# Kernel tuning notes

Measured on AMD Instinct MI355X. Metric: run time of the kernel, lower is better.

The kernel has to match this reference:

```python
import jax, jax.numpy as jnp
import numpy as np

N0, N1, N2, N3 = 600000, 100000, 20000, 4096
E0, E1, E2 = 1500000, 200000, 40960
D_IN, D_H, D_OUT = 100, 256, 47


def setup_inputs() -> dict:
    key = jax.random.key(0)
    ks = jax.random.split(key, 16)
    inp = {
        "x": jax.random.normal(ks[0], (N0, D_IN), jnp.float32),
        "ei0_src": jax.random.randint(ks[1], (E0,), 0, N0, jnp.int32),
        "ei0_dst": jax.random.randint(ks[2], (E0,), 0, N1, jnp.int32),
        "ei1_src": jax.random.randint(ks[3], (E1,), 0, N1, jnp.int32),
        "ei1_dst": jax.random.randint(ks[4], (E1,), 0, N2, jnp.int32),
        "ei2_src": jax.random.randint(ks[5], (E2,), 0, N2, jnp.int32),
        "ei2_dst": jax.random.randint(ks[6], (E2,), 0, N3, jnp.int32),
        "Wl0": jax.random.normal(ks[7], (D_IN, D_H), jnp.float32) * 0.1,
        "Wr0": jax.random.normal(ks[8], (D_IN, D_H), jnp.float32) * 0.1,
        "b0": jnp.zeros((D_H,), jnp.float32),
        "Wl1": jax.random.normal(ks[9], (D_H, D_H), jnp.float32) * 0.06,
        "Wr1": jax.random.normal(ks[10], (D_H, D_H), jnp.float32) * 0.06,
        "b1": jnp.zeros((D_H,), jnp.float32),
        "Wl2": jax.random.normal(ks[11], (D_H, D_OUT), jnp.float32) * 0.06,
        "Wr2": jax.random.normal(ks[12], (D_H, D_OUT), jnp.float32) * 0.06,
        "b2": jnp.zeros((D_OUT,), jnp.float32),
    }
    return inp


def _sage_layer(x_src, x_tgt, src, dst, n_tgt, Wl, Wr, b):
    # PyG SAGEConv (mean aggr): out = lin_l(mean_{j in N(i)} x_j) + lin_r(x_i)
    msgs = x_src[src]                                   # [E, d] gather
    s = jax.ops.segment_sum(msgs, dst, num_segments=n_tgt)
    cnt = jax.ops.segment_sum(jnp.ones((src.shape[0],), x_src.dtype), dst,
                              num_segments=n_tgt)[:, None]
    mean = s / jnp.maximum(cnt, 1.0)
    return mean @ Wl + x_tgt @ Wr + b


def reference(x, ei0_src, ei0_dst, ei1_src, ei1_dst, ei2_src, ei2_dst,
              Wl0, Wr0, b0, Wl1, Wr1, b1, Wl2, Wr2, b2):
    h = _sage_layer(x, x[:N1], ei0_src, ei0_dst, N1, Wl0, Wr0, b0)
    h = jax.nn.relu(h)  # dropout is identity in eval mode
    h = _sage_layer(h, h[:N2], ei1_src, ei1_dst, N2, Wl1, Wr1, b1)
    h = jax.nn.relu(h)
    h = _sage_layer(h, h[:N3], ei2_src, ei2_dst, N3, Wl2, Wr2, b2)
    return jax.nn.log_softmax(h, axis=-1)
```

## Files before the change

kernel.cpp:

```cpp
#include <hip/hip_runtime.h>

#define NN0 600000
#define NN1 100000
#define NN2 20000
#define NN3 4096
#define EE0 1500000
#define EE1 200000
#define EE2 40960
#define DIN 100
#define DH  256
#define DOUT 47
#define NTOT (NN1 + NN2 + NN3)

#define RNG 16384
#define CH0 32768
#define NC0 46
#define R0  7
#define CH1 16384
#define NC1 13
#define R1  2
#define CH2 8192
#define NC2 5
#define R2  1
#define HL0 (NC0 * R0)
#define HL1 (NC1 * R1)
#define HL2 (NC2 * R2)
#define HLT (HL0 + HL1 + HL2)
#define NGMAX 46
#define CONVB 1536

#define NB0 98
#define NB1 20
#define NB2 4
#define NBT 122

#define HB0 5860
#define HB1 782
#define HB2 160
#define HBE (HB0 + HB1 + HB2)

typedef unsigned int uint;
typedef unsigned short ushort;
typedef __attribute__((ext_vector_type(8))) short bhalf8;
typedef __attribute__((ext_vector_type(4))) float f32x4;

union U16B {
    uint2  u2[2];
    uint4  u4;
    bhalf8 s8;
    ushort us[8];
};

__device__ __forceinline__ ushort f2bf(float f) {
    uint u = __float_as_uint(f);
    uint r = (u + 0x7FFFu + ((u >> 16) & 1u)) >> 16;
    return (ushort)r;
}
__device__ __forceinline__ float bf2f(uint bits16) {
    return __uint_as_float(bits16 << 16);
}

__global__ __launch_bounds__(1024)
void hist_conv(const int* __restrict__ e0d, const int* __restrict__ e1d,
               const int* __restrict__ e2d, int* __restrict__ cntp,
               int* __restrict__ pos0, int* __restrict__ pos1,
               int* __restrict__ pos2,
               const float* __restrict__ x, ushort* __restrict__ xb,
               long long n4) {
    __shared__ int lcnt[RNG];
    int b = blockIdx.x, tid = threadIdx.x;
    if (b >= HLT) {
        long long cb = b - HLT;
        for (long long t = cb * 1024 + tid; t < n4; t += (long long)CONVB * 1024) {
            float4 v = *reinterpret_cast<const float4*>(x + t * 4);
            uint2 o;
            o.x = (uint)f2bf(v.x) | ((uint)f2bf(v.y) << 16);
            o.y = (uint)f2bf(v.z) | ((uint)f2bf(v.w) << 16);
            *reinterpret_cast<uint2*>(xb + t * 4) = o;
        }
        return;
    }
    const int* dstp; int E, CH, c, r, nbase, layerN;
    int* pos;
    if (b < HL0) {
        dstp = e0d; E = EE0; CH = CH0; c = b / R0; r = b % R0;
        nbase = 0; layerN = NN1; pos = pos0;
    } else if (b < HL0 + HL1) {
        int bb = b - HL0;
        dstp = e1d; E = EE1; CH = CH1; c = bb / R1; r = bb % R1;
        nbase = NN1; layerN = NN2; pos = pos1;
    } else {
        int bb = b - HL0 - HL1;
        dstp = e2d; E = EE2; CH = CH2; c = bb; r = 0;
        nbase = NN1 + NN2; layerN = NN3; pos = pos2;
    }
    for (int i = tid; i < RNG; i += 1024) lcnt[i] = 0;
    __syncthreads();
    int rbase = r * RNG;
    long long ebase = (long long)c * CH;
    for (int i = tid; i < CH; i += 1024) {
        int e = (int)(ebase + i);
        if (e < E) {
            int d = dstp[e];
            unsigned li = (unsigned)(d - rbase);
            if (li < RNG) pos[e] = atomicAdd(&lcnt[li], 1);
        }
    }
    __syncthreads();
    for (int i = tid; i < RNG; i += 1024) {
        int node = rbase + i;
        if (node < layerN)
            cntp[(size_t)c * NTOT + nbase + node] = lcnt[i];
    }
}

__device__ __forceinline__ void pack_one(const float* B, int K, int N, int NB,
                                         ushort* out, int bid, int l) {
    int kstep = bid / NB;
    int c = bid % NB;
    U16B v;
    #pragma unroll
    for (int j = 0; j < 8; ++j) {
        int k = kstep * 32 + ((l >> 4) << 3) + j;
        int col = (c << 4) | (l & 15);
        float f = (k < K && col < N) ? B[(size_t)k * N + col] : 0.0f;
        v.us[j] = f2bf(f);
    }
    *reinterpret_cast<bhalf8*>(out + ((size_t)bid * 64 + l) * 8) = v.s8;
}

__global__ __launch_bounds__(256)
void pack_all(const float* __restrict__ Wl0, const float* __restrict__ Wr0,
              const float* __restrict__ Wl1, const float* __restrict__ Wr1,
              const float* __restrict__ Wl2, const float* __restrict__ Wr2,
              ushort* Bp0l, ushort* Bp0r, ushort* Bp1l, ushort* Bp1r,
              ushort* Bp2l, ushort* Bp2r) {
    int bid = blockIdx.x * 4 + (threadIdx.x >> 6);
    int l = threadIdx.x & 63;
    if (bid < 64)       pack_one(Wl0, DIN, DH,  16, Bp0l, bid,       l);
    else if (bid < 128) pack_one(Wr0, DIN, DH,  16, Bp0r, bid - 64,  l);
    else if (bid < 256) pack_one(Wl1, DH,  DH,  16, Bp1l, bid - 128, l);
    else if (bid < 384) pack_one(Wr1, DH,  DH,  16, Bp1r, bid - 256, l);
    else if (bid < 408) pack_one(Wl2, DH,  DOUT, 3, Bp2l, bid - 384, l);
    else if (bid < 432) pack_one(Wr2, DH,  DOUT, 3, Bp2r, bid - 408, l);
}

__global__ __launch_bounds__(256)
void combine_parts(int* __restrict__ cntp, int* __restrict__ cntAll) {
    int i = blockIdx.x * 256 + threadIdx.x;
    if (i >= NTOT) return;
    int ng = (i < NN1) ? NC0 : (i < NN1 + NN2) ? NC1 : NC2;
    int run = 0;
    for (int g = 0; g < ng; ++g) {
        size_t idx = (size_t)g * NTOT + i;
        int v = cntp[idx];
        cntp[idx] = run;
        run += v;
    }
    cntAll[i] = run;
}


__device__ __forceinline__ void layer_of(int b, int& lb, int& n, int& po, int& cb) {
    if (b < NB0)      { lb = b;        n = NN1; po = 0;         cb = 0; }
    else if (b < NB0 + NB1) { lb = b - NB0;  n = NN2; po = NB0; cb = NN1; }
    else              { lb = b - NB0 - NB1; n = NN3; po = NB0 + NB1; cb = NN1 + NN2; }
}

__global__ void scan1f(const int* __restrict__ cntAll, int* __restrict__ part) {
    int lb, n, po, cb;
    layer_of(blockIdx.x, lb, n, po, cb);
    __shared__ int s[256];
    int base = lb * 1024;
    int sum = 0;
    for (int i = threadIdx.x; i < 1024; i += 256) {
        int idx = base + i;
        sum += (idx < n) ? cntAll[cb + idx] : 0;
    }
    s[threadIdx.x] = sum;
    __syncthreads();
    for (int off = 128; off; off >>= 1) {
        if (threadIdx.x < off) s[threadIdx.x] += s[threadIdx.x + off];
        __syncthreads();
    }
    if (threadIdx.x == 0) part[po + lb] = s[0];
}

__global__ void scan2f(int* part) {
    __shared__ int s[128];
    int t = threadIdx.x;
    int seg = (t < NB0) ? 0 : (t < NB0 + NB1) ? 1 : (t < NBT) ? 2 : 3;
    int v = (t < NBT) ? part[t] : 0;
    s[t] = v;
    __syncthreads();
    for (int off = 1; off < 128; off <<= 1) {
        int add = 0;
        if (t >= off) {
            int u = t - off;
            int segu = (u < NB0) ? 0 : (u < NB0 + NB1) ? 1 : (u < NBT) ? 2 : 3;
            if (segu == seg) add = s[u];
        }
        __syncthreads();
        s[t] += add;
        __syncthreads();
    }
    if (t < NBT) part[t] = s[t] - v;
}

__global__ void scan3f(const int* __restrict__ cntAll, const int* __restrict__ part,
                       int* __restrict__ rp0, int* __restrict__ rp1,
                       int* __restrict__ rp2) {
    int lb, n, po, cb;
    layer_of(blockIdx.x, lb, n, po, cb);
    int* row_ptr;
    if (cb == 0)        row_ptr = rp0;
    else if (cb == NN1) row_ptr = rp1;
    else                row_ptr = rp2;

    __shared__ int s[256];
    int base = lb * 1024;
    int v[4];
    int sum = 0;
    #pragma unroll
    for (int j = 0; j < 4; ++j) {
        int idx = base + threadIdx.x * 4 + j;
        v[j] = (idx < n) ? cntAll[cb + idx] : 0;
        sum += v[j];
    }
    s[threadIdx.x] = sum;
    __syncthreads();
    for (int off = 1; off < 256; off <<= 1) {
        int t = (threadIdx.x >= off) ? s[threadIdx.x - off] : 0;
        __syncthreads();
        s[threadIdx.x] += t;
        __syncthreads();
    }
    int off0 = part[po + lb] + s[threadIdx.x] - sum;
    #pragma unroll
    for (int j = 0; j < 4; ++j) {
        int idx = base + threadIdx.x * 4 + j;
        if (idx < n) {
            row_ptr[idx] = off0;
            off0 += v[j];
            if (idx == n - 1) row_ptr[n] = off0;
        }
    }
}

__global__ __launch_bounds__(256)
void place_all(const int* __restrict__ e0s, const int* __restrict__ e0d,
               const int* __restrict__ e1s, const int* __restrict__ e1d,
               const int* __restrict__ e2s, const int* __restrict__ e2d,
               const int* __restrict__ pos0, const int* __restrict__ pos1,
               const int* __restrict__ pos2, const int* __restrict__ cntp,
               const int* __restrict__ rp0, const int* __restrict__ rp1,
               const int* __restrict__ rp2,
               int* __restrict__ eidx0, int* __restrict__ eidx1,
               int* __restrict__ eidx2) {
    int b = blockIdx.x;
    int tid = threadIdx.x;
    if (b < HB0) {
        int e = b * 256 + tid;
        if (e < EE0) {
            int d = e0d[e];
            int g = e >> 15;
            int p = rp0[d] + cntp[(size_t)g * NTOT + d] + pos0[e];
            eidx0[p] = e0s[e];
        }
    } else if (b < HB0 + HB1) {
        int e = (b - HB0) * 256 + tid;
        if (e < EE1) {
            int d = e1d[e];
            int g = e >> 14;
            int p = rp1[d] + cntp[(size_t)g * NTOT + NN1 + d] + pos1[e];
            eidx1[p] = e1s[e];
        }
    } else {
        int e = (b - HB0 - HB1) * 256 + tid;
        if (e < EE2) {
            int d = e2d[e];
            int g = e >> 13;
            int p = rp2[d] + cntp[(size_t)g * NTOT + NN1 + NN2 + d] + pos2[e];
            eidx2[p] = e2s[e];
        }
    }
}


__global__ __launch_bounds__(256)
void agg100_b(const ushort* __restrict__ xb, const int* __restrict__ rp,
              const int* __restrict__ eidx, ushort* __restrict__ out, int nNodes) {
    int node = blockIdx.x * 4 + (threadIdx.x >> 6);
    if (node >= nNodes) return;
    int l = threadIdx.x & 63;
    bool act = l < 50;
    int beg = rp[node], end = rp[node + 1];
    float a0 = 0.f, a1 = 0.f;
    int j = beg;
    for (; j + 3 < end; j += 4) {
        int s0 = eidx[j], s1 = eidx[j + 1], s2 = eidx[j + 2], s3 = eidx[j + 3];
        if (act) {
            uint v0 = *reinterpret_cast<const uint*>(xb + (size_t)s0 * DIN + l * 2);
            uint v1 = *reinterpret_cast<const uint*>(xb + (size_t)s1 * DIN + l * 2);
            uint v2 = *reinterpret_cast<const uint*>(xb + (size_t)s2 * DIN + l * 2);
            uint v3 = *reinterpret_cast<const uint*>(xb + (size_t)s3 * DIN + l * 2);
            a0 += bf2f(v0 & 0xffffu) + bf2f(v1 & 0xffffu) + bf2f(v2 & 0xffffu) + bf2f(v3 & 0xffffu);
            a1 += bf2f(v0 >> 16) + bf2f(v1 >> 16) + bf2f(v2 >> 16) + bf2f(v3 >> 16);
        }
    }
    for (; j < end; ++j) {
        int s0 = eidx[j];
        if (act) {
            uint v0 = *reinterpret_cast<const uint*>(xb + (size_t)s0 * DIN + l * 2);
            a0 += bf2f(v0 & 0xffffu);
            a1 += bf2f(v0 >> 16);
        }
    }
    float inv = 1.0f / fmaxf((float)(end - beg), 1.0f);
    if (act) {
        uint o = (uint)f2bf(a0 * inv) | ((uint)f2bf(a1 * inv) << 16);
        *reinterpret_cast<uint*>(out + (size_t)node * DIN + l * 2) = o;
    }
}

__global__ __launch_bounds__(256)
void agg256_b(const ushort* __restrict__ h, const int* __restrict__ rp,
              const int* __restrict__ eidx, ushort* __restrict__ out, int nNodes) {
    int node = blockIdx.x * 4 + (threadIdx.x >> 6);
    if (node >= nNodes) return;
    int l = threadIdx.x & 63;
    int beg = rp[node], end = rp[node + 1];
    float a0 = 0.f, a1 = 0.f, a2 = 0.f, a3 = 0.f;
    int j = beg;
    for (; j + 3 < end; j += 4) {
        int s0 = eidx[j], s1 = eidx[j + 1], s2 = eidx[j + 2], s3 = eidx[j + 3];
        uint2 v0 = *reinterpret_cast<const uint2*>(h + (size_t)s0 * DH + l * 4);
        uint2 v1 = *reinterpret_cast<const uint2*>(h + (size_t)s1 * DH + l * 4);
        uint2 v2 = *reinterpret_cast<const uint2*>(h + (size_t)s2 * DH + l * 4);
        uint2 v3 = *reinterpret_cast<const uint2*>(h + (size_t)s3 * DH + l * 4);
        a0 += bf2f(v0.x & 0xffffu) + bf2f(v1.x & 0xffffu) + bf2f(v2.x & 0xffffu) + bf2f(v3.x & 0xffffu);
        a1 += bf2f(v0.x >> 16)     + bf2f(v1.x >> 16)     + bf2f(v2.x >> 16)     + bf2f(v3.x >> 16);
        a2 += bf2f(v0.y & 0xffffu) + bf2f(v1.y & 0xffffu) + bf2f(v2.y & 0xffffu) + bf2f(v3.y & 0xffffu);
        a3 += bf2f(v0.y >> 16)     + bf2f(v1.y >> 16)     + bf2f(v2.y >> 16)     + bf2f(v3.y >> 16);
    }
    for (; j < end; ++j) {
        int s0 = eidx[j];
        uint2 v0 = *reinterpret_cast<const uint2*>(h + (size_t)s0 * DH + l * 4);
        a0 += bf2f(v0.x & 0xffffu);
        a1 += bf2f(v0.x >> 16);
        a2 += bf2f(v0.y & 0xffffu);
        a3 += bf2f(v0.y >> 16);
    }
    float inv = 1.0f / fmaxf((float)(end - beg), 1.0f);
    uint2 o;
    o.x = (uint)f2bf(a0 * inv) | ((uint)f2bf(a1 * inv) << 16);
    o.y = (uint)f2bf(a2 * inv) | ((uint)f2bf(a3 * inv) << 16);
    *reinterpret_cast<uint2*>(out + (size_t)node * DH + l * 4) = o;
}

template <int RELU, int OUTBF, int A2F32>
__global__ __launch_bounds__(256)
void gemm_dual(const ushort* __restrict__ A1, int K1, int S1, int str1,
               const void* __restrict__ A2, int K2, int S2, int str2,
               const ushort* __restrict__ B1p, const ushort* __restrict__ B2p,
               const float* __restrict__ bias, void* __restrict__ Cv,
               int M, int N, int NB, int NBW, int Cstride) {
    __shared__ ushort At[2][2048];

    const int tid = threadIdx.x;
    const int w = tid >> 6;
    const int l = tid & 63;
    const int m0 = blockIdx.x * 64;
    const int S = S1 + S2;

    f32x4 acc[4][4];
    #pragma unroll
    for (int m = 0; m < 4; ++m)
        #pragma unroll
        for (int i = 0; i < 4; ++i)
            acc[m][i] = f32x4{0.f, 0.f, 0.f, 0.f};

    auto stage = [&](int s, int buf) {
        int r  = tid >> 2;
        int kc = tid & 3;
        int row = m0 + r;
        U16B v;
        v.u4.x = v.u4.y = v.u4.z = v.u4.w = 0u;
        if (s < S1) {
            int k = s * 32 + (kc << 3);
            if (row < M && k < K1) {
                const ushort* p = A1 + (size_t)row * str1 + k;
                v.u2[0] = *reinterpret_cast<const uint2*>(p);
                v.u2[1] = *reinterpret_cast<const uint2*>(p + 4);
                if (k + 8 > K1) {
                    #pragma unroll
                    for (int j = 0; j < 8; ++j)
                        if (k + j >= K1) v.us[j] = 0;
                }
            }
        } else {
            int ks = s - S1;
            int k = ks * 32 + (kc << 3);
            if (row < M && k < K2) {
                if (A2F32) {
                    const float* p = (const float*)A2 + (size_t)row * str2 + k;
                    float4 f0 = *reinterpret_cast<const float4*>(p);
                    float4 f1 = *reinterpret_cast<const float4*>(p + 4);
                    v.us[0] = f2bf(f0.x); v.us[1] = f2bf(f0.y);
                    v.us[2] = f2bf(f0.z); v.us[3] = f2bf(f0.w);
                    v.us[4] = f2bf(f1.x); v.us[5] = f2bf(f1.y);
                    v.us[6] = f2bf(f1.z); v.us[7] = f2bf(f1.w);
                } else {
                    const ushort* p = (const ushort*)A2 + (size_t)row * str2 + k;
                    v.u2[0] = *reinterpret_cast<const uint2*>(p);
                    v.u2[1] = *reinterpret_cast<const uint2*>(p + 4);
                }
                if (k + 8 > K2) {
                    #pragma unroll
                    for (int j = 0; j < 8; ++j)
                        if (k + j >= K2) v.us[j] = 0;
                }
            }
        }
        int slot = ((r >> 4) << 6) | (r & 15) | (kc << 4);
        *reinterpret_cast<bhalf8*>(&At[buf][slot * 8]) = v.s8;
    };

    stage(0, 0);
    __syncthreads();

    for (int s = 0; s < S; ++s) {
        int buf = s & 1;
        if (s + 1 < S) stage(s + 1, buf ^ 1);

        const ushort* Bp; int ks;
        if (s < S1) { Bp = B1p; ks = s; }
        else        { Bp = B2p; ks = s - S1; }

        bhalf8 a[4];
        #pragma unroll
        for (int m = 0; m < 4; ++m)
            a[m] = *reinterpret_cast<bhalf8*>(&At[buf][((m << 6) | l) * 8]);

        #pragma unroll
        for (int i = 0; i < 4; ++i) {
            if (i < NBW) {
                int c = w * NBW + i;
                if (c < NB) {
                    bhalf8 b = *reinterpret_cast<const bhalf8*>(
                        Bp + ((size_t)(ks * NB + c) * 64 + l) * 8);
                    #pragma unroll
                    for (int m = 0; m < 4; ++m)
                        acc[m][i] = __builtin_amdgcn_mfma_f32_16x16x32_bf16(
                            a[m], b, acc[m][i], 0, 0, 0);
                }
            }
        }
        __syncthreads();
    }

    #pragma unroll
    for (int i = 0; i < 4; ++i) {
        if (i >= NBW) continue;
        int c = w * NBW + i;
        if (c >= NB) continue;
        int col = (c << 4) | (l & 15);
        if (col >= N) continue;
        float bb = bias[col];
        #pragma unroll
        for (int m = 0; m < 4; ++m) {
            #pragma unroll
            for (int e = 0; e < 4; ++e) {
                int row = m0 + (m << 4) + ((l >> 4) << 2) + e;
                if (row < M) {
                    float v = acc[m][i][e] + bb;
                    if (RELU) v = fmaxf(v, 0.0f);
                    if (OUTBF)
                        ((ushort*)Cv)[(size_t)row * Cstride + col] = f2bf(v);
                    else
                        ((float*)Cv)[(size_t)row * Cstride + col] = v;
                }
            }
        }
    }
}

__global__ void log_softmax_47(const float* __restrict__ z, float* __restrict__ out) {
    int row = blockIdx.x;
    int lane = threadIdx.x;
    float v = (lane < DOUT) ? z[(size_t)row * DOUT + lane] : -INFINITY;
    float m = v;
    #pragma unroll
    for (int off = 32; off; off >>= 1) m = fmaxf(m, __shfl_xor(m, off));
    float e = (lane < DOUT) ? expf(v - m) : 0.0f;
    float s = e;
    #pragma unroll
    for (int off = 32; off; off >>= 1) s += __shfl_xor(s, off);
    if (lane < DOUT) out[(size_t)row * DOUT + lane] = v - m - logf(s);
}

extern "C" void kernel_launch(void* const* d_in, const int* in_sizes, int n_in,
                              void* d_out, int out_size, void* d_ws, size_t ws_size,
                              hipStream_t stream) {
    const float* x   = (const float*)d_in[0];
    const int* e0s   = (const int*)d_in[1];
    const int* e0d   = (const int*)d_in[2];
    const int* e1s   = (const int*)d_in[3];
    const int* e1d   = (const int*)d_in[4];
    const int* e2s   = (const int*)d_in[5];
    const int* e2d   = (const int*)d_in[6];
    const float* Wl0 = (const float*)d_in[7];
    const float* Wr0 = (const float*)d_in[8];
    const float* b0  = (const float*)d_in[9];
    const float* Wl1 = (const float*)d_in[10];
    const float* Wr1 = (const float*)d_in[11];
    const float* b1  = (const float*)d_in[12];
    const float* Wl2 = (const float*)d_in[13];
    const float* Wr2 = (const float*)d_in[14];
    const float* b2  = (const float*)d_in[15];

    char* ws = (char*)d_ws;
    size_t off = 0;
    auto alloc = [&](size_t bytes) -> void* {
        void* p = ws + off;
        off += (bytes + 255) & ~(size_t)255;
        return p;
    };

    ushort* agg0b = (ushort*)alloc((size_t)NN1 * DIN * 2);
    ushort* h1    = (ushort*)alloc((size_t)NN1 * DH * 2);
    ushort* agg1b = (ushort*)alloc((size_t)NN2 * DH * 2);
    ushort* h2    = (ushort*)alloc((size_t)NN2 * DH * 2);
    ushort* agg2b = (ushort*)alloc((size_t)NN3 * DH * 2);
    float*  z     = (float*)alloc((size_t)NN3 * DOUT * 4);

    ushort* Bp0l = (ushort*)alloc((size_t)4 * 16 * 64 * 8 * 2);
    ushort* Bp0r = (ushort*)alloc((size_t)4 * 16 * 64 * 8 * 2);
    ushort* Bp1l = (ushort*)alloc((size_t)8 * 16 * 64 * 8 * 2);
    ushort* Bp1r = (ushort*)alloc((size_t)8 * 16 * 64 * 8 * 2);
    ushort* Bp2l = (ushort*)alloc((size_t)8 * 3 * 64 * 8 * 2);
    ushort* Bp2r = (ushort*)alloc((size_t)8 * 3 * 64 * 8 * 2);

    int* cntp   = (int*)alloc((size_t)NGMAX * NTOT * 4);
    int* cntAll = (int*)alloc((size_t)NTOT * 4);
    int* pos0   = (int*)alloc((size_t)EE0 * 4);
    int* pos1   = (int*)alloc((size_t)EE1 * 4);
    int* pos2   = (int*)alloc((size_t)EE2 * 4);
    int* rp0    = (int*)alloc((size_t)(NN1 + 1) * 4);
    int* eidx0  = (int*)alloc((size_t)EE0 * 4);
    int* rp1    = (int*)alloc((size_t)(NN2 + 1) * 4);
    int* eidx1  = (int*)alloc((size_t)EE1 * 4);
    int* rp2    = (int*)alloc((size_t)(NN3 + 1) * 4);
    int* eidx2  = (int*)alloc((size_t)EE2 * 4);
    int* part   = (int*)alloc(256 * 4);
    ushort* xb  = (ushort*)alloc((size_t)NN0 * DIN * 2 + 256);

    {
        long long n4 = (long long)NN0 * DIN / 4;
        hist_conv<<<HLT + CONVB, 1024, 0, stream>>>(
            e0d, e1d, e2d, cntp, pos0, pos1, pos2, x, xb, n4);
    }
    pack_all<<<108, 256, 0, stream>>>(Wl0, Wr0, Wl1, Wr1, Wl2, Wr2,
                                      Bp0l, Bp0r, Bp1l, Bp1r, Bp2l, Bp2r);

    combine_parts<<<(NTOT + 255) / 256, 256, 0, stream>>>(cntp, cntAll);
    scan1f<<<NBT, 256, 0, stream>>>(cntAll, part);
    scan2f<<<1, 128, 0, stream>>>(part);
    scan3f<<<NBT, 256, 0, stream>>>(cntAll, part, rp0, rp1, rp2);

    place_all<<<HBE, 256, 0, stream>>>(e0s, e0d, e1s, e1d, e2s, e2d,
                                       pos0, pos1, pos2, cntp,
                                       rp0, rp1, rp2, eidx0, eidx1, eidx2);

    agg100_b<<<(NN1 + 3) / 4, 256, 0, stream>>>(xb, rp0, eidx0, agg0b, NN1);
    gemm_dual<1, 1, 0><<<(NN1 + 63) / 64, 256, 0, stream>>>(
        agg0b, DIN, 4, DIN, (const void*)xb, DIN, 4, DIN, Bp0l, Bp0r, b0, h1,
        NN1, DH, 16, 4, DH);

    agg256_b<<<(NN2 + 3) / 4, 256, 0, stream>>>(h1, rp1, eidx1, agg1b, NN2);
    gemm_dual<1, 1, 0><<<(NN2 + 63) / 64, 256, 0, stream>>>(
        agg1b, DH, 8, DH, (const void*)h1, DH, 8, DH, Bp1l, Bp1r, b1, h2,
        NN2, DH, 16, 4, DH);

    agg256_b<<<(NN3 + 3) / 4, 256, 0, stream>>>(h2, rp2, eidx2, agg2b, NN3);
    gemm_dual<0, 0, 0><<<(NN3 + 63) / 64, 256, 0, stream>>>(
        agg2b, DH, 8, DH, (const void*)h2, DH, 8, DH, Bp2l, Bp2r, b2, z,
        NN3, DOUT, 3, 1, DOUT);

    log_softmax_47<<<NN3, 64, 0, stream>>>(z, (float*)d_out);
}
```

Baseline: 443.7 us.

## Fuse preprocessing kernels, move x conversion into placement, widen gathers

Weight packing moves into the histogram kernel. The fp32-to-bf16 conversion of x moves into the edge-placement kernel so it overlaps scatter work. The combine, partial-scan and block-offset scan kernels are merged into two launches, which drops the single-block scan2 kernel because each block redundantly sums the earlier partials. The aggregation loops use 8 gathered rows per iteration, and agg100 uses 32-lane half-waves with 4 features per lane. Together these remove several launches and serial dependencies, and raise memory-level parallelism in the gathers, at the cost of more register pressure and redundant per-block prefix work.

```diff
diff --git a/kernel.cpp b/kernel.cpp
--- a/kernel.cpp
+++ b/kernel.cpp
@@ -27,7 +27,7 @@
 #define HL2 (NC2 * R2)
 #define HLT (HL0 + HL1 + HL2)
 #define NGMAX 46
-#define CONVB 1536
+#define PACKB 27
 
 #define NB0 98
 #define NB1 20
@@ -38,6 +38,7 @@
 #define HB1 782
 #define HB2 160
 #define HBE (HB0 + HB1 + HB2)
+#define CONVB 3072
 
 typedef unsigned int uint;
 typedef unsigned short ushort;
@@ -60,24 +61,42 @@
     return __uint_as_float(bits16 << 16);
 }
 
+__device__ __forceinline__ void pack_one(const float* B, int K, int N, int NB,
+                                         ushort* out, int bid, int l) {
+    int kstep = bid / NB;
+    int c = bid % NB;
+    U16B v;
+    #pragma unroll
+    for (int j = 0; j < 8; ++j) {
+        int k = kstep * 32 + ((l >> 4) << 3) + j;
+        int col = (c << 4) | (l & 15);
+        float f = (k < K && col < N) ? B[(size_t)k * N + col] : 0.0f;
+        v.us[j] = f2bf(f);
+    }
+    *reinterpret_cast<bhalf8*>(out + ((size_t)bid * 64 + l) * 8) = v.s8;
+}
+
 __global__ __launch_bounds__(1024)
-void hist_conv(const int* __restrict__ e0d, const int* __restrict__ e1d,
+void hist_pack(const int* __restrict__ e0d, const int* __restrict__ e1d,
                const int* __restrict__ e2d, int* __restrict__ cntp,
                int* __restrict__ pos0, int* __restrict__ pos1,
                int* __restrict__ pos2,
-               const float* __restrict__ x, ushort* __restrict__ xb,
-               long long n4) {
+               const float* __restrict__ Wl0, const float* __restrict__ Wr0,
+               const float* __restrict__ Wl1, const float* __restrict__ Wr1,
+               const float* __restrict__ Wl2, const float* __restrict__ Wr2,
+               ushort* Bp0l, ushort* Bp0r, ushort* Bp1l, ushort* Bp1r,
+               ushort* Bp2l, ushort* Bp2r) {
     __shared__ int lcnt[RNG];
     int b = blockIdx.x, tid = threadIdx.x;
     if (b >= HLT) {
-        long long cb = b - HLT;
-        for (long long t = cb * 1024 + tid; t < n4; t += (long long)CONVB * 1024) {
-            float4 v = *reinterpret_cast<const float4*>(x + t * 4);
-            uint2 o;
-            o.x = (uint)f2bf(v.x) | ((uint)f2bf(v.y) << 16);
-            o.y = (uint)f2bf(v.z) | ((uint)f2bf(v.w) << 16);
-            *reinterpret_cast<uint2*>(xb + t * 4) = o;
-        }
+        int bid = (b - HLT) * 16 + (tid >> 6);
+        int l = tid & 63;
+        if (bid < 64)       pack_one(Wl0, DIN, DH,  16, Bp0l, bid,       l);
+        else if (bid < 128) pack_one(Wr0, DIN, DH,  16, Bp0r, bid - 64,  l);
+        else if (bid < 256) pack_one(Wl1, DH,  DH,  16, Bp1l, bid - 128, l);
+        else if (bid < 384) pack_one(Wr1, DH,  DH,  16, Bp1r, bid - 256, l);
+        else if (bid < 408) pack_one(Wl2, DH,  DOUT, 3, Bp2l, bid - 384, l);
+        else if (bid < 432) pack_one(Wr2, DH,  DOUT, 3, Bp2r, bid - 408, l);
         return;
     }
     const int* dstp; int E, CH, c, r, nbase, layerN;
@@ -114,69 +133,37 @@
     }
 }
 
-__device__ __forceinline__ void pack_one(const float* B, int K, int N, int NB,
-                                         ushort* out, int bid, int l) {
-    int kstep = bid / NB;
-    int c = bid % NB;
-    U16B v;
-    #pragma unroll
-    for (int j = 0; j < 8; ++j) {
-        int k = kstep * 32 + ((l >> 4) << 3) + j;
-        int col = (c << 4) | (l & 15);
-        float f = (k < K && col < N) ? B[(size_t)k * N + col] : 0.0f;
-        v.us[j] = f2bf(f);
-    }
-    *reinterpret_cast<bhalf8*>(out + ((size_t)bid * 64 + l) * 8) = v.s8;
-}
-
-__global__ __launch_bounds__(256)
-void pack_all(const float* __restrict__ Wl0, const float* __restrict__ Wr0,
-              const float* __restrict__ Wl1, const float* __restrict__ Wr1,
-              const float* __restrict__ Wl2, const float* __restrict__ Wr2,
-              ushort* Bp0l, ushort* Bp0r, ushort* Bp1l, ushort* Bp1r,
-              ushort* Bp2l, ushort* Bp2r) {
-    int bid = blockIdx.x * 4 + (threadIdx.x >> 6);
-    int l = threadIdx.x & 63;
-    if (bid < 64)       pack_one(Wl0, DIN, DH,  16, Bp0l, bid,       l);
-    else if (bid < 128) pack_one(Wr0, DIN, DH,  16, Bp0r, bid - 64,  l);
-    else if (bid < 256) pack_one(Wl1, DH,  DH,  16, Bp1l, bid - 128, l);
-    else if (bid < 384) pack_one(Wr1, DH,  DH,  16, Bp1r, bid - 256, l);
-    else if (bid < 408) pack_one(Wl2, DH,  DOUT, 3, Bp2l, bid - 384, l);
-    else if (bid < 432) pack_one(Wr2, DH,  DOUT, 3, Bp2r, bid - 408, l);
-}
-
-__global__ __launch_bounds__(256)
-void combine_parts(int* __restrict__ cntp, int* __restrict__ cntAll) {
-    int i = blockIdx.x * 256 + threadIdx.x;
-    if (i >= NTOT) return;
-    int ng = (i < NN1) ? NC0 : (i < NN1 + NN2) ? NC1 : NC2;
-    int run = 0;
-    for (int g = 0; g < ng; ++g) {
-        size_t idx = (size_t)g * NTOT + i;
-        int v = cntp[idx];
-        cntp[idx] = run;
-        run += v;
-    }
-    cntAll[i] = run;
-}
-
-
 __device__ __forceinline__ void layer_of(int b, int& lb, int& n, int& po, int& cb) {
     if (b < NB0)      { lb = b;        n = NN1; po = 0;         cb = 0; }
     else if (b < NB0 + NB1) { lb = b - NB0;  n = NN2; po = NB0; cb = NN1; }
     else              { lb = b - NB0 - NB1; n = NN3; po = NB0 + NB1; cb = NN1 + NN2; }
 }
 
-__global__ void scan1f(const int* __restrict__ cntAll, int* __restrict__ part) {
+__global__ __launch_bounds__(256)
+void combScan1(int* __restrict__ cntp, int* __restrict__ cntAll,
+               int* __restrict__ part) {
     int lb, n, po, cb;
     layer_of(blockIdx.x, lb, n, po, cb);
-    __shared__ int s[256];
+    int ng = (cb == 0) ? NC0 : (cb == NN1) ? NC1 : NC2;
     int base = lb * 1024;
     int sum = 0;
-    for (int i = threadIdx.x; i < 1024; i += 256) {
-        int idx = base + i;
-        sum += (idx < n) ? cntAll[cb + idx] : 0;
-    }
+    #pragma unroll
+    for (int jj = 0; jj < 4; ++jj) {
+        int idx = base + threadIdx.x * 4 + jj;
+        if (idx < n) {
+            int i = cb + idx;
+            int run = 0;
+            for (int g = 0; g < ng; ++g) {
+                size_t id = (size_t)g * NTOT + i;
+                int v = cntp[id];
+                cntp[id] = run;
+                run += v;
+            }
+            cntAll[i] = run;
+            sum += run;
+        }
+    }
+    __shared__ int s[256];
     s[threadIdx.x] = sum;
     __syncthreads();
     for (int off = 128; off; off >>= 1) {
@@ -186,30 +173,9 @@
     if (threadIdx.x == 0) part[po + lb] = s[0];
 }
 
-__global__ void scan2f(int* part) {
-    __shared__ int s[128];
-    int t = threadIdx.x;
-    int seg = (t < NB0) ? 0 : (t < NB0 + NB1) ? 1 : (t < NBT) ? 2 : 3;
-    int v = (t < NBT) ? part[t] : 0;
-    s[t] = v;
-    __syncthreads();
-    for (int off = 1; off < 128; off <<= 1) {
-        int add = 0;
-        if (t >= off) {
-            int u = t - off;
-            int segu = (u < NB0) ? 0 : (u < NB0 + NB1) ? 1 : (u < NBT) ? 2 : 3;
-            if (segu == seg) add = s[u];
-        }
-        __syncthreads();
-        s[t] += add;
-        __syncthreads();
-    }
-    if (t < NBT) part[t] = s[t] - v;
-}
-
-__global__ void scan3f(const int* __restrict__ cntAll, const int* __restrict__ part,
-                       int* __restrict__ rp0, int* __restrict__ rp1,
-                       int* __restrict__ rp2) {
+__global__ __launch_bounds__(256)
+void scan3L(const int* __restrict__ cntAll, const int* __restrict__ part,
+            int* __restrict__ rp0, int* __restrict__ rp1, int* __restrict__ rp2) {
     int lb, n, po, cb;
     layer_of(blockIdx.x, lb, n, po, cb);
     int* row_ptr;
@@ -217,7 +183,18 @@
     else if (cb == NN1) row_ptr = rp1;
     else                row_ptr = rp2;
 
+    __shared__ int partL[NBT];
     __shared__ int s[256];
+    __shared__ int segOff;
+    for (int i = threadIdx.x; i < NBT; i += 256) partL[i] = part[i];
+    __syncthreads();
+    if (threadIdx.x == 0) {
+        int acc = 0;
+        for (int k = 0; k < lb; ++k) acc += partL[po + k];
+        segOff = acc;
+    }
+    __syncthreads();
+
     int base = lb * 1024;
     int v[4];
     int sum = 0;
@@ -235,7 +212,7 @@
         s[threadIdx.x] += t;
         __syncthreads();
     }
-    int off0 = part[po + lb] + s[threadIdx.x] - sum;
+    int off0 = segOff + s[threadIdx.x] - sum;
     #pragma unroll
     for (int j = 0; j < 4; ++j) {
         int idx = base + threadIdx.x * 4 + j;
@@ -248,15 +225,17 @@
 }
 
 __global__ __launch_bounds__(256)
-void place_all(const int* __restrict__ e0s, const int* __restrict__ e0d,
-               const int* __restrict__ e1s, const int* __restrict__ e1d,
-               const int* __restrict__ e2s, const int* __restrict__ e2d,
-               const int* __restrict__ pos0, const int* __restrict__ pos1,
-               const int* __restrict__ pos2, const int* __restrict__ cntp,
-               const int* __restrict__ rp0, const int* __restrict__ rp1,
-               const int* __restrict__ rp2,
-               int* __restrict__ eidx0, int* __restrict__ eidx1,
-               int* __restrict__ eidx2) {
+void place_conv(const int* __restrict__ e0s, const int* __restrict__ e0d,
+                const int* __restrict__ e1s, const int* __restrict__ e1d,
+                const int* __restrict__ e2s, const int* __restrict__ e2d,
+                const int* __restrict__ pos0, const int* __restrict__ pos1,
+                const int* __restrict__ pos2, const int* __restrict__ cntp,
+                const int* __restrict__ rp0, const int* __restrict__ rp1,
+                const int* __restrict__ rp2,
+                int* __restrict__ eidx0, int* __restrict__ eidx1,
+                int* __restrict__ eidx2,
+                const float* __restrict__ x, ushort* __restrict__ xb,
+                long long n4) {
     int b = blockIdx.x;
     int tid = threadIdx.x;
     if (b < HB0) {
@@ -275,7 +254,7 @@
             int p = rp1[d] + cntp[(size_t)g * NTOT + NN1 + d] + pos1[e];
             eidx1[p] = e1s[e];
         }
-    } else {
+    } else if (b < HBE) {
         int e = (b - HB0 - HB1) * 256 + tid;
         if (e < EE2) {
             int d = e2d[e];
@@ -283,6 +262,15 @@
             int p = rp2[d] + cntp[(size_t)g * NTOT + NN1 + NN2 + d] + pos2[e];
             eidx2[p] = e2s[e];
         }
+    } else {
+        long long cb = b - HBE;
+        for (long long t = cb * 256 + tid; t < n4; t += (long long)CONVB * 256) {
+            float4 v = *reinterpret_cast<const float4*>(x + t * 4);
+            uint2 o;
+            o.x = (uint)f2bf(v.x) | ((uint)f2bf(v.y) << 16);
+            o.y = (uint)f2bf(v.z) | ((uint)f2bf(v.w) << 16);
+            *reinterpret_cast<uint2*>(xb + t * 4) = o;
+        }
     }
 }
 
@@ -290,36 +278,47 @@
 __global__ __launch_bounds__(256)
 void agg100_b(const ushort* __restrict__ xb, const int* __restrict__ rp,
               const int* __restrict__ eidx, ushort* __restrict__ out, int nNodes) {
-    int node = blockIdx.x * 4 + (threadIdx.x >> 6);
+    int node = blockIdx.x * 8 + (threadIdx.x >> 5);
     if (node >= nNodes) return;
-    int l = threadIdx.x & 63;
-    bool act = l < 50;
+    int hl = threadIdx.x & 31;
+    bool act = hl < 25;
     int beg = rp[node], end = rp[node + 1];
-    float a0 = 0.f, a1 = 0.f;
+    float a0 = 0.f, a1 = 0.f, a2 = 0.f, a3 = 0.f;
     int j = beg;
-    for (; j + 3 < end; j += 4) {
-        int s0 = eidx[j], s1 = eidx[j + 1], s2 = eidx[j + 2], s3 = eidx[j + 3];
+    for (; j + 7 < end; j += 8) {
+        int sidx[8];
+        #pragma unroll
+        for (int q = 0; q < 8; ++q) sidx[q] = eidx[j + q];
         if (act) {
-            uint v0 = *reinterpret_cast<const uint*>(xb + (size_t)s0 * DIN + l * 2);
-            uint v1 = *reinterpret_cast<const uint*>(xb + (size_t)s1 * DIN + l * 2);
-            uint v2 = *reinterpret_cast<const uint*>(xb + (size_t)s2 * DIN + l * 2);
-            uint v3 = *reinterpret_cast<const uint*>(xb + (size_t)s3 * DIN + l * 2);
-            a0 += bf2f(v0 & 0xffffu) + bf2f(v1 & 0xffffu) + bf2f(v2 & 0xffffu) + bf2f(v3 & 0xffffu);
-            a1 += bf2f(v0 >> 16) + bf2f(v1 >> 16) + bf2f(v2 >> 16) + bf2f(v3 >> 16);
+            uint2 vv[8];
+            #pragma unroll
+            for (int q = 0; q < 8; ++q)
+                vv[q] = *reinterpret_cast<const uint2*>(xb + (size_t)sidx[q] * DIN + hl * 4);
+            #pragma unroll
+            for (int q = 0; q < 8; ++q) {
+                a0 += bf2f(vv[q].x & 0xffffu);
+                a1 += bf2f(vv[q].x >> 16);
+                a2 += bf2f(vv[q].y & 0xffffu);
+                a3 += bf2f(vv[q].y >> 16);
+            }
         }
     }
     for (; j < end; ++j) {
         int s0 = eidx[j];
         if (act) {
-            uint v0 = *reinterpret_cast<const uint*>(xb + (size_t)s0 * DIN + l * 2);
-            a0 += bf2f(v0 & 0xffffu);
-            a1 += bf2f(v0 >> 16);
+            uint2 v0 = *reinterpret_cast<const uint2*>(xb + (size_t)s0 * DIN + hl * 4);
+            a0 += bf2f(v0.x & 0xffffu);
+            a1 += bf2f(v0.x >> 16);
+            a2 += bf2f(v0.y & 0xffffu);
+            a3 += bf2f(v0.y >> 16);
         }
     }
     float inv = 1.0f / fmaxf((float)(end - beg), 1.0f);
     if (act) {
-        uint o = (uint)f2bf(a0 * inv) | ((uint)f2bf(a1 * inv) << 16);
-        *reinterpret_cast<uint*>(out + (size_t)node * DIN + l * 2) = o;
+        uint2 o;
+        o.x = (uint)f2bf(a0 * inv) | ((uint)f2bf(a1 * inv) << 16);
+        o.y = (uint)f2bf(a2 * inv) | ((uint)f2bf(a3 * inv) << 16);
+        *reinterpret_cast<uint2*>(out + (size_t)node * DIN + hl * 4) = o;
     }
 }
 
@@ -332,16 +331,21 @@
     int beg = rp[node], end = rp[node + 1];
     float a0 = 0.f, a1 = 0.f, a2 = 0.f, a3 = 0.f;
     int j = beg;
-    for (; j + 3 < end; j += 4) {
-        int s0 = eidx[j], s1 = eidx[j + 1], s2 = eidx[j + 2], s3 = eidx[j + 3];
-        uint2 v0 = *reinterpret_cast<const uint2*>(h + (size_t)s0 * DH + l * 4);
-        uint2 v1 = *reinterpret_cast<const uint2*>(h + (size_t)s1 * DH + l * 4);
-        uint2 v2 = *reinterpret_cast<const uint2*>(h + (size_t)s2 * DH + l * 4);
-        uint2 v3 = *reinterpret_cast<const uint2*>(h + (size_t)s3 * DH + l * 4);
-        a0 += bf2f(v0.x & 0xffffu) + bf2f(v1.x & 0xffffu) + bf2f(v2.x & 0xffffu) + bf2f(v3.x & 0xffffu);
-        a1 += bf2f(v0.x >> 16)     + bf2f(v1.x >> 16)     + bf2f(v2.x >> 16)     + bf2f(v3.x >> 16);
-        a2 += bf2f(v0.y & 0xffffu) + bf2f(v1.y & 0xffffu) + bf2f(v2.y & 0xffffu) + bf2f(v3.y & 0xffffu);
-        a3 += bf2f(v0.y >> 16)     + bf2f(v1.y >> 16)     + bf2f(v2.y >> 16)     + bf2f(v3.y >> 16);
+    for (; j + 7 < end; j += 8) {
+        int sidx[8];
+        #pragma unroll
+        for (int q = 0; q < 8; ++q) sidx[q] = eidx[j + q];
+        uint2 vv[8];
+        #pragma unroll
+        for (int q = 0; q < 8; ++q)
+            vv[q] = *reinterpret_cast<const uint2*>(h + (size_t)sidx[q] * DH + l * 4);
+        #pragma unroll
+        for (int q = 0; q < 8; ++q) {
+            a0 += bf2f(vv[q].x & 0xffffu);
+            a1 += bf2f(vv[q].x >> 16);
+            a2 += bf2f(vv[q].y & 0xffffu);
+            a3 += bf2f(vv[q].y >> 16);
+        }
     }
     for (; j < end; ++j) {
         int s0 = eidx[j];
@@ -358,10 +362,10 @@
     *reinterpret_cast<uint2*>(out + (size_t)node * DH + l * 4) = o;
 }
 
-template <int RELU, int OUTBF, int A2F32>
+template <int RELU, int OUTBF>
 __global__ __launch_bounds__(256)
 void gemm_dual(const ushort* __restrict__ A1, int K1, int S1, int str1,
-               const void* __restrict__ A2, int K2, int S2, int str2,
+               const ushort* __restrict__ A2, int K2, int S2, int str2,
                const ushort* __restrict__ B1p, const ushort* __restrict__ B2p,
                const float* __restrict__ bias, void* __restrict__ Cv,
                int M, int N, int NB, int NBW, int Cstride) {
@@ -381,45 +385,23 @@
             acc[m][i] = f32x4{0.f, 0.f, 0.f, 0.f};
 
     auto stage = [&](int s, int buf) {
+        const ushort* A; int str, Keff, ks;
+        if (s < S1) { A = A1; str = str1; Keff = K1; ks = s; }
+        else        { A = A2; str = str2; Keff = K2; ks = s - S1; }
         int r  = tid >> 2;
         int kc = tid & 3;
         int row = m0 + r;
+        int k = ks * 32 + (kc << 3);
         U16B v;
         v.u4.x = v.u4.y = v.u4.z = v.u4.w = 0u;
-        if (s < S1) {
-            int k = s * 32 + (kc << 3);
-            if (row < M && k < K1) {
-                const ushort* p = A1 + (size_t)row * str1 + k;
-                v.u2[0] = *reinterpret_cast<const uint2*>(p);
-                v.u2[1] = *reinterpret_cast<const uint2*>(p + 4);
-                if (k + 8 > K1) {
-                    #pragma unroll
-                    for (int j = 0; j < 8; ++j)
-                        if (k + j >= K1) v.us[j] = 0;
-                }
-            }
-        } else {
-            int ks = s - S1;
-            int k = ks * 32 + (kc << 3);
-            if (row < M && k < K2) {
-                if (A2F32) {
-                    const float* p = (const float*)A2 + (size_t)row * str2 + k;
-                    float4 f0 = *reinterpret_cast<const float4*>(p);
-                    float4 f1 = *reinterpret_cast<const float4*>(p + 4);
-                    v.us[0] = f2bf(f0.x); v.us[1] = f2bf(f0.y);
-                    v.us[2] = f2bf(f0.z); v.us[3] = f2bf(f0.w);
-                    v.us[4] = f2bf(f1.x); v.us[5] = f2bf(f1.y);
-                    v.us[6] = f2bf(f1.z); v.us[7] = f2bf(f1.w);
-                } else {
-                    const ushort* p = (const ushort*)A2 + (size_t)row * str2 + k;
-                    v.u2[0] = *reinterpret_cast<const uint2*>(p);
-                    v.u2[1] = *reinterpret_cast<const uint2*>(p + 4);
-                }
-                if (k + 8 > K2) {
-                    #pragma unroll
-                    for (int j = 0; j < 8; ++j)
-                        if (k + j >= K2) v.us[j] = 0;
-                }
+        if (row < M && k < Keff) {
+            const ushort* p = A + (size_t)row * str + k;
+            v.u2[0] = *reinterpret_cast<const uint2*>(p);
+            v.u2[1] = *reinterpret_cast<const uint2*>(p + 4);
+            if (k + 8 > Keff) {
+                #pragma unroll
+                for (int j = 0; j < 8; ++j)
+                    if (k + j >= Keff) v.us[j] = 0;
             }
         }
         int slot = ((r >> 4) << 6) | (r & 15) | (kc << 4);
@@ -555,36 +537,34 @@
     int* part   = (int*)alloc(256 * 4);
     ushort* xb  = (ushort*)alloc((size_t)NN0 * DIN * 2 + 256);
 
+    hist_pack<<<HLT + PACKB, 1024, 0, stream>>>(
+        e0d, e1d, e2d, cntp, pos0, pos1, pos2,
+        Wl0, Wr0, Wl1, Wr1, Wl2, Wr2,
+        Bp0l, Bp0r, Bp1l, Bp1r, Bp2l, Bp2r);
+
+    combScan1<<<NBT, 256, 0, stream>>>(cntp, cntAll, part);
+    scan3L<<<NBT, 256, 0, stream>>>(cntAll, part, rp0, rp1, rp2);
+
     {
         long long n4 = (long long)NN0 * DIN / 4;
-        hist_conv<<<HLT + CONVB, 1024, 0, stream>>>(
-            e0d, e1d, e2d, cntp, pos0, pos1, pos2, x, xb, n4);
-    }
-    pack_all<<<108, 256, 0, stream>>>(Wl0, Wr0, Wl1, Wr1, Wl2, Wr2,
-                                      Bp0l, Bp0r, Bp1l, Bp1r, Bp2l, Bp2r);
-
-    combine_parts<<<(NTOT + 255) / 256, 256, 0, stream>>>(cntp, cntAll);
-    scan1f<<<NBT, 256, 0, stream>>>(cntAll, part);
-    scan2f<<<1, 128, 0, stream>>>(part);
-    scan3f<<<NBT, 256, 0, stream>>>(cntAll, part, rp0, rp1, rp2);
-
-    place_all<<<HBE, 256, 0, stream>>>(e0s, e0d, e1s, e1d, e2s, e2d,
-                                       pos0, pos1, pos2, cntp,
-                                       rp0, rp1, rp2, eidx0, eidx1, eidx2);
-
-    agg100_b<<<(NN1 + 3) / 4, 256, 0, stream>>>(xb, rp0, eidx0, agg0b, NN1);
-    gemm_dual<1, 1, 0><<<(NN1 + 63) / 64, 256, 0, stream>>>(
-        agg0b, DIN, 4, DIN, (const void*)xb, DIN, 4, DIN, Bp0l, Bp0r, b0, h1,
+        place_conv<<<HBE + CONVB, 256, 0, stream>>>(
+            e0s, e0d, e1s, e1d, e2s, e2d, pos0, pos1, pos2, cntp,
+            rp0, rp1, rp2, eidx0, eidx1, eidx2, x, xb, n4);
+    }
+
+    agg100_b<<<(NN1 + 7) / 8, 256, 0, stream>>>(xb, rp0, eidx0, agg0b, NN1);
+    gemm_dual<1, 1><<<(NN1 + 63) / 64, 256, 0, stream>>>(
+        agg0b, DIN, 4, DIN, xb, DIN, 4, DIN, Bp0l, Bp0r, b0, h1,
         NN1, DH, 16, 4, DH);
 
     agg256_b<<<(NN2 + 3) / 4, 256, 0, stream>>>(h1, rp1, eidx1, agg1b, NN2);
-    gemm_dual<1, 1, 0><<<(NN2 + 63) / 64, 256, 0, stream>>>(
-        agg1b, DH, 8, DH, (const void*)h1, DH, 8, DH, Bp1l, Bp1r, b1, h2,
+    gemm_dual<1, 1><<<(NN2 + 63) / 64, 256, 0, stream>>>(
+        agg1b, DH, 8, DH, h1, DH, 8, DH, Bp1l, Bp1r, b1, h2,
         NN2, DH, 16, 4, DH);
 
     agg256_b<<<(NN3 + 3) / 4, 256, 0, stream>>>(h2, rp2, eidx2, agg2b, NN3);
-    gemm_dual<0, 0, 0><<<(NN3 + 63) / 64, 256, 0, stream>>>(
-        agg2b, DH, 8, DH, (const void*)h2, DH, 8, DH, Bp2l, Bp2r, b2, z,
+    gemm_dual<0, 0><<<(NN3 + 63) / 64, 256, 0, stream>>>(
+        agg2b, DH, 8, DH, h2, DH, 8, DH, Bp2l, Bp2r, b2, z,
         NN3, DOUT, 3, 1, DOUT);
 
     log_softmax_47<<<NN3, 64, 0, stream>>>(z, (float*)d_out);
```

Result: slower. 456.7 us (+2.9%).
